# Performance work log

Hardware: AMD Instinct MI355X
Metric: run time of the kernel (lower is better)

## Reference

```python
import jax, jax.numpy as jnp
import numpy as np

BLOCK_K = 128  # per_1x128 block quantization: block_n=1 (per row), block_k=128


def _dequant(wq, scale):
    # wq: [E, N, K] quantized codes; scale: [E, N, ceil(K/BLOCK_K)]
    K = wq.shape[-1]
    s_full = jnp.repeat(scale, BLOCK_K, axis=-1)[..., :K]
    return wq * s_full


def setup_inputs() -> dict:
    key = jax.random.key(0)
    ks = jax.random.split(key, 6)
    T, E, H, I = 1024, 8, 1024, 768
    x = jax.random.normal(ks[0], (T, H), dtype=jnp.float32)
    router_logits = jax.random.normal(ks[1], (T, E), dtype=jnp.float32)
    # fp8 codes simulated as float values; block scales positive (scale_inv)
    w13_weight = jax.random.normal(ks[2], (E, 2 * I, H), dtype=jnp.float32) * 0.05
    w13_weight_scale_inv = jax.random.uniform(ks[3], (E, 2 * I, H // BLOCK_K), dtype=jnp.float32, minval=0.5, maxval=1.5)
    w2_weight = jax.random.normal(ks[4], (E, H, I), dtype=jnp.float32) * 0.05
    w2_weight_scale_inv = jax.random.uniform(ks[5], (E, H, I // BLOCK_K), dtype=jnp.float32, minval=0.5, maxval=1.5)
    return {
        "x": x,
        "router_logits": router_logits,
        "w13_weight": w13_weight,
        "w13_weight_scale_inv": w13_weight_scale_inv,
        "w2_weight": w2_weight,
        "w2_weight_scale_inv": w2_weight_scale_inv,
        "top_k": 2,
    }


def reference(x, router_logits, w13_weight, w13_weight_scale_inv, w2_weight, w2_weight_scale_inv, top_k):
    T, H = x.shape
    E = router_logits.shape[-1]
    I = w2_weight.shape[-1]

    # ---- dequantize block-scaled weights (inline dequant of fp8 grouped GEMM) ----
    w13 = _dequant(w13_weight, w13_weight_scale_inv)   # [E, 2I, H]
    w2 = _dequant(w2_weight, w2_weight_scale_inv)      # [E, H, I]

    # ---- routing: softmax scoring, top_k, renormalize ----
    probs = jax.nn.softmax(router_logits, axis=-1)     # [T, E]
    topk_w, topk_idx = jax.lax.top_k(probs, top_k)     # [T, K]
    topk_w = topk_w / jnp.sum(topk_w, axis=-1, keepdims=True)  # renormalize=True
    # dense combine weights [T, E] (scatter of top_k routing weights)
    combine = jnp.zeros((T, E), x.dtype).at[jnp.arange(T)[:, None], topk_idx].add(topk_w)

    # ---- grouped expert FFN (dense-over-experts reference) ----
    gate_up = jnp.einsum('th,enh->ten', x, w13)        # [T, E, 2I]
    gate, up = gate_up[..., :I], gate_up[..., I:]
    act = jax.nn.silu(gate) * up                       # silu activation ('silu')
    out_e = jnp.einsum('tei,ehi->teh', act, w2)        # [T, E, H]

    # ---- combine ----
    return jnp.einsum('teh,te->th', out_e, combine)    # [T, H]
```

## Files before the change

kernel.cpp:

```cpp
#include <hip/hip_runtime.h>

#define T_TOK 1024
#define H_DIM 1024
#define I_DIM 768
#define E_NUM 8

#define G13 1572864
#define G2   786432
#define GX   131072
#define GTOT 2621440
#define GHALF 1310720

typedef __bf16 bf16x8 __attribute__((ext_vector_type(8)));
typedef float  f32x4  __attribute__((ext_vector_type(4)));

__device__ inline bf16x8 cvt8(float4 a, float4 b, float s) {
    bf16x8 o;
    o[0] = (__bf16)(a.x * s); o[1] = (__bf16)(a.y * s);
    o[2] = (__bf16)(a.z * s); o[3] = (__bf16)(a.w * s);
    o[4] = (__bf16)(b.x * s); o[5] = (__bf16)(b.y * s);
    o[6] = (__bf16)(b.z * s); o[7] = (__bf16)(b.w * s);
    return o;
}

__device__ inline void prep_group(
    int g,
    const float* __restrict__ w13, const float* __restrict__ w13s,
    const float* __restrict__ w2,  const float* __restrict__ w2s,
    const float* __restrict__ x,   float4* __restrict__ out4,
    __bf16* __restrict__ w13d, __bf16* __restrict__ w2d, __bf16* __restrict__ xbf)
{
    if (g < G13) {
        int k8 = g & 127;
        int row = g >> 7;
        float s = w13s[(row << 3) | (k8 >> 4)];
        const float4* src = (const float4*)w13 + (size_t)g * 2;
        *(bf16x8*)(w13d + (size_t)g * 8) = cvt8(src[0], src[1], s);
    } else if (g < G13 + G2) {
        int g2 = g - G13;
        unsigned row = (unsigned)g2 / 96u;
        int k8 = g2 - row * 96;
        float s = w2s[row * 6 + (k8 >> 4)];
        const float4* src = (const float4*)w2 + (size_t)g2 * 2;
        *(bf16x8*)(w2d + (size_t)g2 * 8) = cvt8(src[0], src[1], s);
    } else if (g < G13 + G2 + GX) {
        int gx = g - (G13 + G2);
        const float4* src = (const float4*)x + (size_t)gx * 2;
        *(bf16x8*)(xbf + (size_t)gx * 8) = cvt8(src[0], src[1], 1.0f);
    } else {
        int go = g - (G13 + G2 + GX);
        float4 z = make_float4(0.f, 0.f, 0.f, 0.f);
        out4[2 * go] = z; out4[2 * go + 1] = z;
    }
}

__global__ __launch_bounds__(256) void prep_kernel(
    const float* __restrict__ w13, const float* __restrict__ w13s,
    const float* __restrict__ w2,  const float* __restrict__ w2s,
    const float* __restrict__ x,   float4* __restrict__ out4,
    __bf16* __restrict__ w13d, __bf16* __restrict__ w2d, __bf16* __restrict__ xbf,
    const float* __restrict__ logits,
    int* __restrict__ counts, int* __restrict__ base,
    int* __restrict__ tok_list, float* __restrict__ wt_list)
{
    const int bx = blockIdx.x, tid = threadIdx.x;
    if (bx < 5120) {
        int g0 = bx * 256 + tid;
        prep_group(g0, w13, w13s, w2, w2s, x, out4, w13d, w2d, xbf);
        prep_group(g0 + GHALF, w13, w13s, w2, w2s, x, out4, w13d, w2d, xbf);
        return;
    }
    __shared__ int cnt[E_NUM];
    if (tid < E_NUM) cnt[tid] = 0;
    __syncthreads();
#pragma unroll
    for (int tt = 0; tt < 4; tt++) {
        int t = tid + tt * 256;
        float l[E_NUM];
#pragma unroll
        for (int e = 0; e < E_NUM; e++) l[e] = logits[t * E_NUM + e];
        int e0 = 0; float m0 = l[0];
#pragma unroll
        for (int e = 1; e < E_NUM; e++) if (l[e] > m0) { m0 = l[e]; e0 = e; }
        int e1 = -1; float m1 = -3e38f;
#pragma unroll
        for (int e = 0; e < E_NUM; e++) if (e != e0 && l[e] > m1) { m1 = l[e]; e1 = e; }
        float w0 = 1.0f / (1.0f + expf(m1 - m0));
        float w1 = 1.0f - w0;
        int p0 = atomicAdd(&cnt[e0], 1);
        tok_list[e0 * T_TOK + p0] = t;
        wt_list[e0 * T_TOK + p0] = w0;
        int p1 = atomicAdd(&cnt[e1], 1);
        tok_list[e1 * T_TOK + p1] = t;
        wt_list[e1 * T_TOK + p1] = w1;
    }
    __syncthreads();
    if (tid == 0) {
        int s = 0;
        for (int e = 0; e < E_NUM; e++) { base[e] = s; counts[e] = cnt[e]; s += cnt[e]; }
    }
}

#define MFMA(A, B, C) __builtin_amdgcn_mfma_f32_16x16x32_bf16(A, B, C, 0, 0, 0)

struct StA { uint4 a0, a1; };
struct StB { uint4 b0, b1, b2, b3; };

__device__ inline StA ldA(const __bf16* pA0, const __bf16* pA1, int k) {
    StA s;
    s.a0 = *(const uint4*)(pA0 + k);
    s.a1 = *(const uint4*)(pA1 + k);
    return s;
}
__device__ inline StB ldB(const __bf16* pB, int k) {
    StB s;
    s.b0 = *(const uint4*)(pB + k);
    s.b1 = *(const uint4*)(pB + k + 8);
    s.b2 = *(const uint4*)(pB + k + 16);
    s.b3 = *(const uint4*)(pB + k + 24);
    return s;
}
__device__ inline void stA(char* As, int aw0, int aw1, const StA& s) {
    *(uint4*)(As + aw0) = s.a0;
    *(uint4*)(As + aw1) = s.a1;
}
__device__ inline void stB(char* Bs, int bw0, int bw1, int bw2, int bw3, const StB& s) {
    *(uint4*)(Bs + bw0) = s.b0;
    *(uint4*)(Bs + bw1) = s.b1;
    *(uint4*)(Bs + bw2) = s.b2;
    *(uint4*)(Bs + bw3) = s.b3;
}

__global__ __launch_bounds__(256, 3) void gemm1_kernel(
    const __bf16* __restrict__ xbf,
    const __bf16* __restrict__ w13d,
    const int* __restrict__ counts,
    const int* __restrict__ base,
    const int* __restrict__ tok_list,
    __bf16* __restrict__ act)
{
    const int bx = blockIdx.x;
    const int xcd = bx & 7, t = bx >> 3;
    const int p = t % 12, m = t / 12;
    const int P = xcd + 8 * p;
    const int nb = P % 12, e = P / 12;
    const int count = counts[e];
    const int m0 = m * 64;
    if (m0 >= count) return;
    const int n0 = nb * 64;
    const int abase = base[e];

    __shared__ union {
        struct { __bf16 Bs[2][128 * 64]; __bf16 As[2][64 * 64]; } s;
        float gu[64 * 132];
    } u;
    __shared__ int tokS[64];

    const int tid = threadIdx.x;
    if (tid < 64) {
        int r = m0 + tid;
        tokS[tid] = (r < count) ? tok_list[e * T_TOK + r] : tok_list[e * T_TOK];
    }

    const int brow = tid >> 1, bg0 = (tid & 1) * 4;
    const int nB = (brow < 64) ? (n0 + brow) : (I_DIM + n0 + brow - 64);
    const __bf16* pB = w13d + ((size_t)e * 2 * I_DIM + nB) * H_DIM + bg0 * 8;
    const int bw0 = brow * 128 + (((bg0 + 0) ^ (brow & 7)) << 4);
    const int bw1 = brow * 128 + (((bg0 + 1) ^ (brow & 7)) << 4);
    const int bw2 = brow * 128 + (((bg0 + 2) ^ (brow & 7)) << 4);
    const int bw3 = brow * 128 + (((bg0 + 3) ^ (brow & 7)) << 4);

    StB XB = ldB(pB, 0);
    StB YB = ldB(pB, 64);
    __syncthreads();

    const int arow = tid >> 3, ag = tid & 7;
    const __bf16* pA0 = xbf + (size_t)tokS[arow] * H_DIM + ag * 8;
    const __bf16* pA1 = xbf + (size_t)tokS[arow + 32] * H_DIM + ag * 8;
    const int aw0 = arow * 128 + ((ag ^ (arow & 7)) << 4);
    const int aw1 = aw0 + 32 * 128;

    StA XA = ldA(pA0, pA1, 0);
    StA YA = ldA(pA0, pA1, 64);

    const int wid = tid >> 6, lane = tid & 63, lrow = lane & 15, quad = lane >> 4;
    int aoff[2][4], boff[2][2];
#pragma unroll
    for (int kk = 0; kk < 2; kk++) {
        int gph = ((kk * 4 + quad) ^ (lrow & 7)) << 4;
#pragma unroll
        for (int i = 0; i < 4; i++) aoff[kk][i] = (i * 16 + lrow) * 128 + gph;
#pragma unroll
        for (int j = 0; j < 2; j++) boff[kk][j] = (wid * 32 + j * 16 + lrow) * 128 + gph;
    }

    f32x4 acc[4][2];
#pragma unroll
    for (int i = 0; i < 4; i++)
#pragma unroll
        for (int j = 0; j < 2; j++) { f32x4 z = {0.f, 0.f, 0.f, 0.f}; acc[i][j] = z; }

    char* A0 = (char*)u.s.As[0]; char* A1 = (char*)u.s.As[1];
    char* B0 = (char*)u.s.Bs[0]; char* B1 = (char*)u.s.Bs[1];

    auto compute = [&](const char* Ab, const char* Bb) {
#pragma unroll
        for (int kk = 0; kk < 2; kk++) {
            bf16x8 b0 = *(const bf16x8*)(Bb + boff[kk][0]);
            bf16x8 b1 = *(const bf16x8*)(Bb + boff[kk][1]);
#pragma unroll
            for (int i = 0; i < 4; i++) {
                bf16x8 a = *(const bf16x8*)(Ab + aoff[kk][i]);
                acc[i][0] = MFMA(a, b0, acc[i][0]);
                acc[i][1] = MFMA(a, b1, acc[i][1]);
            }
        }
    };

    stA(A0, aw0, aw1, XA); stB(B0, bw0, bw1, bw2, bw3, XB);
    XA = ldA(pA0, pA1, 128); XB = ldB(pB, 128);
    __syncthreads();

#pragma unroll
    for (int uu = 0; uu < 8; ++uu) {
        stA(A1, aw0, aw1, YA); stB(B1, bw0, bw1, bw2, bw3, YB);
        if (2 * uu + 3 < 16) { YA = ldA(pA0, pA1, (2 * uu + 3) * 64); YB = ldB(pB, (2 * uu + 3) * 64); }
        compute(A0, B0);
        __syncthreads();
        if (uu < 7) { stA(A0, aw0, aw1, XA); stB(B0, bw0, bw1, bw2, bw3, XB); }
        if (2 * uu + 4 < 16) { XA = ldA(pA0, pA1, (2 * uu + 4) * 64); XB = ldB(pB, (2 * uu + 4) * 64); }
        compute(A1, B1);
        __syncthreads();
    }

#pragma unroll
    for (int i = 0; i < 4; i++)
#pragma unroll
        for (int j = 0; j < 2; j++)
#pragma unroll
            for (int r = 0; r < 4; r++) {
                int mr = i * 16 + quad * 4 + r;
                int c = wid * 32 + j * 16 + lrow;
                u.gu[mr * 132 + c] = acc[i][j][r];
            }
    __syncthreads();

#pragma unroll
    for (int ii = 0; ii < 16; ii++) {
        int o = ii * 256 + tid;
        int mr = o >> 6, c = o & 63;
        if (m0 + mr < count) {
            float g  = u.gu[mr * 132 + c];
            float up = u.gu[mr * 132 + 64 + c];
            float a  = g / (1.0f + expf(-g)) * up;
            act[(size_t)(abase + m0 + mr) * I_DIM + n0 + c] = (__bf16)a;
        }
    }
}

__global__ __launch_bounds__(256, 3) void gemm2_kernel(
    const __bf16* __restrict__ act,
    const __bf16* __restrict__ w2d,
    const int* __restrict__ counts,
    const int* __restrict__ base,
    const int* __restrict__ tok_list,
    const float* __restrict__ wt_list,
    float* __restrict__ out)
{
    const int bx = blockIdx.x;
    const int xcd = bx & 7, t = bx >> 3;
    const int kh = t & 1;
    const int t2 = t >> 1;
    const int p = t2 & 7, m = t2 >> 3;
    const int P = xcd + 8 * p;
    const int nb = P & 7, e = P >> 3;
    const int count = counts[e];
    const int m0 = m * 64;
    if (m0 >= count) return;
    const int n0 = nb * 128;
    const int abase = base[e];
    const int kb = kh * 384;

    __shared__ struct { __bf16 Bs[2][128 * 64]; __bf16 As[2][64 * 64]; } s;

    const int tid = threadIdx.x;
    const int arow = tid >> 3, ag = tid & 7;
    int gr0 = abase + m0 + arow;      if (gr0 > 2 * T_TOK - 1) gr0 = 2 * T_TOK - 1;
    int gr1 = abase + m0 + arow + 32; if (gr1 > 2 * T_TOK - 1) gr1 = 2 * T_TOK - 1;
    const __bf16* pA0 = act + (size_t)gr0 * I_DIM + kb + ag * 8;
    const __bf16* pA1 = act + (size_t)gr1 * I_DIM + kb + ag * 8;
    const int aw0 = arow * 128 + ((ag ^ (arow & 7)) << 4);
    const int aw1 = aw0 + 32 * 128;

    const int brow = tid >> 1, bg0 = (tid & 1) * 4;
    const __bf16* pB = w2d + ((size_t)e * H_DIM + n0 + brow) * I_DIM + kb + bg0 * 8;
    const int bw0 = brow * 128 + (((bg0 + 0) ^ (brow & 7)) << 4);
    const int bw1 = brow * 128 + (((bg0 + 1) ^ (brow & 7)) << 4);
    const int bw2 = brow * 128 + (((bg0 + 2) ^ (brow & 7)) << 4);
    const int bw3 = brow * 128 + (((bg0 + 3) ^ (brow & 7)) << 4);

    const int wid = tid >> 6, lane = tid & 63, lrow = lane & 15, quad = lane >> 4;
    int aoff[2][4], boff[2][2];
#pragma unroll
    for (int kk = 0; kk < 2; kk++) {
        int gph = ((kk * 4 + quad) ^ (lrow & 7)) << 4;
#pragma unroll
        for (int i = 0; i < 4; i++) aoff[kk][i] = (i * 16 + lrow) * 128 + gph;
#pragma unroll
        for (int j = 0; j < 2; j++) boff[kk][j] = (wid * 32 + j * 16 + lrow) * 128 + gph;
    }

    f32x4 acc[4][2];
#pragma unroll
    for (int i = 0; i < 4; i++)
#pragma unroll
        for (int j = 0; j < 2; j++) { f32x4 z = {0.f, 0.f, 0.f, 0.f}; acc[i][j] = z; }

    char* A0 = (char*)s.As[0]; char* A1 = (char*)s.As[1];
    char* B0 = (char*)s.Bs[0]; char* B1 = (char*)s.Bs[1];

    auto compute = [&](const char* Ab, const char* Bb) {
#pragma unroll
        for (int kk = 0; kk < 2; kk++) {
            bf16x8 b0 = *(const bf16x8*)(Bb + boff[kk][0]);
            bf16x8 b1 = *(const bf16x8*)(Bb + boff[kk][1]);
#pragma unroll
            for (int i = 0; i < 4; i++) {
                bf16x8 a = *(const bf16x8*)(Ab + aoff[kk][i]);
                acc[i][0] = MFMA(a, b0, acc[i][0]);
                acc[i][1] = MFMA(a, b1, acc[i][1]);
            }
        }
    };

    StA XA = ldA(pA0, pA1, 0);
    StB XB = ldB(pB, 0);
    StA YA = ldA(pA0, pA1, 64);
    StB YB = ldB(pB, 64);
    stA(A0, aw0, aw1, XA); stB(B0, bw0, bw1, bw2, bw3, XB);
    XA = ldA(pA0, pA1, 128); XB = ldB(pB, 128);
    __syncthreads();

#pragma unroll
    for (int uu = 0; uu < 3; ++uu) {
        stA(A1, aw0, aw1, YA); stB(B1, bw0, bw1, bw2, bw3, YB);
        if (2 * uu + 3 < 6) { YA = ldA(pA0, pA1, (2 * uu + 3) * 64); YB = ldB(pB, (2 * uu + 3) * 64); }
        compute(A0, B0);
        __syncthreads();
        if (uu < 2) { stA(A0, aw0, aw1, XA); stB(B0, bw0, bw1, bw2, bw3, XB); }
        if (2 * uu + 4 < 6) { XA = ldA(pA0, pA1, (2 * uu + 4) * 64); XB = ldB(pB, (2 * uu + 4) * 64); }
        compute(A1, B1);
        __syncthreads();
    }

#pragma unroll
    for (int i = 0; i < 4; i++)
#pragma unroll
        for (int r = 0; r < 4; r++) {
            int mr = i * 16 + quad * 4 + r;
            if (m0 + mr < count) {
                int   tk = tok_list[e * T_TOK + m0 + mr];
                float w  = wt_list[e * T_TOK + m0 + mr];
#pragma unroll
                for (int j = 0; j < 2; j++) {
                    int h = n0 + wid * 32 + j * 16 + lrow;
                    atomicAdd(&out[(size_t)tk * H_DIM + h], w * acc[i][j][r]);
                }
            }
        }
}

extern "C" void kernel_launch(void* const* d_in, const int* in_sizes, int n_in,
                              void* d_out, int out_size, void* d_ws, size_t ws_size,
                              hipStream_t stream) {
    (void)in_sizes; (void)n_in; (void)out_size; (void)ws_size;
    const float* x      = (const float*)d_in[0];
    const float* logits = (const float*)d_in[1];
    const float* w13    = (const float*)d_in[2];
    const float* w13s   = (const float*)d_in[3];
    const float* w2     = (const float*)d_in[4];
    const float* w2s    = (const float*)d_in[5];
    float* out = (float*)d_out;

    char* ws = (char*)d_ws;
    int*    counts   = (int*)ws;
    int*    base     = (int*)(ws + 128);
    int*    tok_list = (int*)(ws + 256);
    float*  wt_list  = (float*)(ws + 256 + 32768);
    __bf16* act      = (__bf16*)(ws + 65792);
    __bf16* xbf      = (__bf16*)(ws + 65792 + 3145728);
    __bf16* w13d     = (__bf16*)(ws + 65792 + 3145728 + 2097152);
    __bf16* w2d      = (__bf16*)(ws + 65792 + 3145728 + 2097152 + 25165824);

    prep_kernel<<<dim3(5121), 256, 0, stream>>>(
        w13, w13s, w2, w2s, x, (float4*)out, w13d, w2d, xbf,
        logits, counts, base, tok_list, wt_list);
    gemm1_kernel<<<dim3(1536), 256, 0, stream>>>(
        xbf, w13d, counts, base, tok_list, act);
    gemm2_kernel<<<dim3(2048), 256, 0, stream>>>(
        act, w2d, counts, base, tok_list, wt_list, out);
}
```

Baseline: 157.3 us.

## Move w2 dequant and output zeroing into gemm1 launch to overlap with GEMM

The w2 dequantization and output zeroing move out of the prep kernel into extra blocks of the gemm1 launch, so they run alongside the first grouped GEMM instead of before it. Prep now handles only the w13 dequant, the x conversion and routing. The intent is to shorten the serial prep phase and fill idle CUs during gemm1, which has many early-exiting blocks. The risk is that the extra memory-bound blocks compete for bandwidth with the gemm1 tiles.

```diff
diff --git a/kernel.cpp b/kernel.cpp
--- a/kernel.cpp
+++ b/kernel.cpp
@@ -8,8 +8,6 @@
 #define G13 1572864
 #define G2   786432
 #define GX   131072
-#define GTOT 2621440
-#define GHALF 1310720
 
 typedef __bf16 bf16x8 __attribute__((ext_vector_type(8)));
 typedef float  f32x4  __attribute__((ext_vector_type(4)));
@@ -23,51 +21,48 @@
     return o;
 }
 
-__device__ inline void prep_group(
-    int g,
+__device__ inline void w13_group(int g, const float* __restrict__ w13,
+                                 const float* __restrict__ w13s,
+                                 __bf16* __restrict__ w13d) {
+    int k8 = g & 127;
+    int row = g >> 7;
+    float s = w13s[(row << 3) | (k8 >> 4)];
+    const float4* src = (const float4*)w13 + (size_t)g * 2;
+    *(bf16x8*)(w13d + (size_t)g * 8) = cvt8(src[0], src[1], s);
+}
+
+__device__ inline void w2_group(int g2, const float* __restrict__ w2,
+                                const float* __restrict__ w2s,
+                                __bf16* __restrict__ w2d) {
+    unsigned row = (unsigned)g2 / 96u;
+    int k8 = g2 - row * 96;
+    float s = w2s[row * 6 + (k8 >> 4)];
+    const float4* src = (const float4*)w2 + (size_t)g2 * 2;
+    *(bf16x8*)(w2d + (size_t)g2 * 8) = cvt8(src[0], src[1], s);
+}
+
+__global__ __launch_bounds__(256) void prep1_kernel(
     const float* __restrict__ w13, const float* __restrict__ w13s,
-    const float* __restrict__ w2,  const float* __restrict__ w2s,
-    const float* __restrict__ x,   float4* __restrict__ out4,
-    __bf16* __restrict__ w13d, __bf16* __restrict__ w2d, __bf16* __restrict__ xbf)
-{
-    if (g < G13) {
-        int k8 = g & 127;
-        int row = g >> 7;
-        float s = w13s[(row << 3) | (k8 >> 4)];
-        const float4* src = (const float4*)w13 + (size_t)g * 2;
-        *(bf16x8*)(w13d + (size_t)g * 8) = cvt8(src[0], src[1], s);
-    } else if (g < G13 + G2) {
-        int g2 = g - G13;
-        unsigned row = (unsigned)g2 / 96u;
-        int k8 = g2 - row * 96;
-        float s = w2s[row * 6 + (k8 >> 4)];
-        const float4* src = (const float4*)w2 + (size_t)g2 * 2;
-        *(bf16x8*)(w2d + (size_t)g2 * 8) = cvt8(src[0], src[1], s);
-    } else if (g < G13 + G2 + GX) {
-        int gx = g - (G13 + G2);
-        const float4* src = (const float4*)x + (size_t)gx * 2;
-        *(bf16x8*)(xbf + (size_t)gx * 8) = cvt8(src[0], src[1], 1.0f);
-    } else {
-        int go = g - (G13 + G2 + GX);
-        float4 z = make_float4(0.f, 0.f, 0.f, 0.f);
-        out4[2 * go] = z; out4[2 * go + 1] = z;
-    }
-}
-
-__global__ __launch_bounds__(256) void prep_kernel(
-    const float* __restrict__ w13, const float* __restrict__ w13s,
-    const float* __restrict__ w2,  const float* __restrict__ w2s,
-    const float* __restrict__ x,   float4* __restrict__ out4,
-    __bf16* __restrict__ w13d, __bf16* __restrict__ w2d, __bf16* __restrict__ xbf,
-    const float* __restrict__ logits,
+    const float* __restrict__ x,   const float* __restrict__ logits,
+    __bf16* __restrict__ w13d,     __bf16* __restrict__ xbf,
     int* __restrict__ counts, int* __restrict__ base,
     int* __restrict__ tok_list, float* __restrict__ wt_list)
 {
     const int bx = blockIdx.x, tid = threadIdx.x;
-    if (bx < 5120) {
-        int g0 = bx * 256 + tid;
-        prep_group(g0, w13, w13s, w2, w2s, x, out4, w13d, w2d, xbf);
-        prep_group(g0 + GHALF, w13, w13s, w2, w2s, x, out4, w13d, w2d, xbf);
+    if (bx < 3072) {
+        int g0 = bx * 512 + tid;
+        w13_group(g0, w13, w13s, w13d);
+        w13_group(g0 + 256, w13, w13s, w13d);
+        return;
+    }
+    if (bx < 3328) {
+        int gx = (bx - 3072) * 512 + tid;
+#pragma unroll
+        for (int q = 0; q < 2; q++) {
+            int g = gx + q * 256;
+            const float4* src = (const float4*)x + (size_t)g * 2;
+            *(bf16x8*)(xbf + (size_t)g * 8) = cvt8(src[0], src[1], 1.0f);
+        }
         return;
     }
     __shared__ int cnt[E_NUM];
@@ -137,9 +132,25 @@
     const int* __restrict__ counts,
     const int* __restrict__ base,
     const int* __restrict__ tok_list,
-    __bf16* __restrict__ act)
+    __bf16* __restrict__ act,
+    const float* __restrict__ w2, const float* __restrict__ w2s,
+    __bf16* __restrict__ w2d, float4* __restrict__ out4)
 {
     const int bx = blockIdx.x;
+    const int tid = threadIdx.x;
+    if (bx >= 1536) {
+        if (bx < 3072) {
+            int g0 = (bx - 1536) * 512 + tid;
+            w2_group(g0, w2, w2s, w2d);
+            w2_group(g0 + 256, w2, w2s, w2d);
+        } else {
+            int i0 = (bx - 3072) * 512 + tid;
+            float4 z = make_float4(0.f, 0.f, 0.f, 0.f);
+            out4[i0] = z; out4[i0 + 256] = z;
+        }
+        return;
+    }
+
     const int xcd = bx & 7, t = bx >> 3;
     const int p = t % 12, m = t / 12;
     const int P = xcd + 8 * p;
@@ -156,7 +167,6 @@
     } u;
     __shared__ int tokS[64];
 
-    const int tid = threadIdx.x;
     if (tid < 64) {
         int r = m0 + tid;
         tokS[tid] = (r < count) ? tok_list[e * T_TOK + r] : tok_list[e * T_TOK];
@@ -392,11 +402,10 @@
     __bf16* w13d     = (__bf16*)(ws + 65792 + 3145728 + 2097152);
     __bf16* w2d      = (__bf16*)(ws + 65792 + 3145728 + 2097152 + 25165824);
 
-    prep_kernel<<<dim3(5121), 256, 0, stream>>>(
-        w13, w13s, w2, w2s, x, (float4*)out, w13d, w2d, xbf,
-        logits, counts, base, tok_list, wt_list);
-    gemm1_kernel<<<dim3(1536), 256, 0, stream>>>(
-        xbf, w13d, counts, base, tok_list, act);
+    prep1_kernel<<<dim3(3329), 256, 0, stream>>>(
+        w13, w13s, x, logits, w13d, xbf, counts, base, tok_list, wt_list);
+    gemm1_kernel<<<dim3(3328), 256, 0, stream>>>(
+        xbf, w13d, counts, base, tok_list, act, w2, w2s, w2d, (float4*)out);
     gemm2_kernel<<<dim3(2048), 256, 0, stream>>>(
         act, w2d, counts, base, tok_list, wt_list, out);
 }
```

After: 156.9 us. No clear change (-0.3%).
